# Optimization experiments

Measured on AMD Instinct MI355X. Metric: run time of the kernel, lower is better.

Reference implementation:

```python
import jax, jax.numpy as jnp
import numpy as np

N, E, F_IN, F_OUT = 20000, 8192, 128, 128


def setup_inputs() -> dict:
    key = jax.random.key(0)
    k1, k2, k3, k4, k5 = jax.random.split(key, 5)
    x = jax.random.normal(k1, (N, F_IN), dtype=jnp.float32)
    H = jax.random.uniform(k2, (N, E), dtype=jnp.float32)
    W = jax.random.uniform(k3, (E,), dtype=jnp.float32)  # diagonal of hyperedge weight matrix
    lin_w = jax.random.normal(k4, (F_OUT, F_IN), dtype=jnp.float32) * (1.0 / np.sqrt(F_IN))
    lin_b = jax.random.normal(k5, (F_OUT,), dtype=jnp.float32) * 0.01
    return {"x": x, "H": H, "W": W, "lin_w": lin_w, "lin_b": lin_b}


def reference(x, H, W, lin_w, lin_b):
    # Degrees
    Dv = jnp.clip(jnp.sum(H, axis=1), 1.0, None)          # [N] node degrees
    De = jnp.clip(jnp.sum(H, axis=0), 1.0, None)          # [E] hyperedge degrees
    dv_inv_sqrt = Dv ** -0.5                               # diag(Dv^-1/2)
    de_inv = 1.0 / De                                      # diag(De^-1)
    # Linear projection of node features
    xw = x @ lin_w.T + lin_b                               # [N, F_OUT]
    # L @ xw computed right-to-left: Dv^-1/2 H W De^-1 H^T Dv^-1/2 xw
    t = H.T @ (dv_inv_sqrt[:, None] * xw)                  # [E, F_OUT]
    t = (W * de_inv)[:, None] * t                          # diagonal W and De^-1 scaling
    out = dv_inv_sqrt[:, None] * (H @ t)                   # [N, F_OUT]
    return jax.nn.gelu(out, approximate=False)             # torch F.gelu default = exact erf
```

## Files before the change

kernel.cpp:

```cpp
#include <hip/hip_runtime.h>
#include <math.h>

static constexpr int N = 20000;
static constexpr int E = 8192;
static constexpr int F = 128;
static constexpr int NP = 20480;
static constexpr int NP2 = 20096;
static constexpr int PREP_BLOCKS = 2048;
static constexpr int XW_BLOCKS = NP / 8;
static constexpr int KS_B = 8;
static constexpr int KS_C = 4;

typedef short bf16x8 __attribute__((ext_vector_type(8)));
typedef float f32x4 __attribute__((ext_vector_type(4)));

__device__ __forceinline__ float gelu_erf(float x) {
    return 0.5f * x * (1.0f + erff(x * 0.70710678118654752440f));
}
__device__ __forceinline__ unsigned f2bf(float f) {
    unsigned u = __float_as_uint(f);
    return (u + 0x7FFFu + ((u >> 16) & 1u)) >> 16;
}
__device__ __forceinline__ void gload16(const void* g, void* lds) {
    __builtin_amdgcn_global_load_lds(
        (const __attribute__((address_space(1))) unsigned int*)g,
        (__attribute__((address_space(3))) unsigned int*)lds, 16, 0, 0);
}

__global__ __launch_bounds__(256, 8) void k_prep(const float* __restrict__ H,
                                                 float* __restrict__ Dv,
                                                 ushort* __restrict__ Hbs) {
    __shared__ float rp[10][4];
    const int tid = threadIdx.x, lane = tid & 63, wid = tid >> 6;
    const int r0 = blockIdx.x * 10;
    if (r0 >= N) {
        uint4 z = make_uint4(0, 0, 0, 0);
        for (int r = 0; r < 10; ++r) {
            ushort* orow = Hbs + (size_t)(r0 + r) * E;
#pragma unroll
            for (int j = 0; j < 4; ++j) *(uint4*)(orow + (j * 256 + tid) * 8) = z;
        }
        return;
    }
    for (int r = 0; r < 10; ++r) {
        const float* row = H + (size_t)(r0 + r) * E;
        ushort* orow = Hbs + (size_t)(r0 + r) * E;
        float rs = 0.f;
#pragma unroll
        for (int j = 0; j < 4; ++j) {
            const float* base = row + (j * 256 + tid) * 8;
            float4 va = *(const float4*)(base);
            float4 vb = *(const float4*)(base + 4);
            rs += (va.x + va.y) + (va.z + va.w);
            rs += (vb.x + vb.y) + (vb.z + vb.w);
            uint4 o;
            o.x = f2bf(va.x) | (f2bf(va.y) << 16);
            o.y = f2bf(va.z) | (f2bf(va.w) << 16);
            o.z = f2bf(vb.x) | (f2bf(vb.y) << 16);
            o.w = f2bf(vb.z) | (f2bf(vb.w) << 16);
            *(uint4*)(orow + (j * 256 + tid) * 8) = o;
        }
#pragma unroll
        for (int off = 32; off > 0; off >>= 1) rs += __shfl_xor(rs, off, 64);
        if (lane == 0) rp[r][wid] = rs;
    }
    __syncthreads();
    if (tid < 10) Dv[r0 + tid] = rp[tid][0] + rp[tid][1] + rp[tid][2] + rp[tid][3];
}

__global__ __launch_bounds__(256) void k_xw(const float* __restrict__ x,
                                            const float* __restrict__ lin_w,
                                            const float* __restrict__ lin_b,
                                            const float* __restrict__ Dv,
                                            ushort* __restrict__ yT) {
    __shared__ __align__(16) char smem[4096];
    const int tid = threadIdx.x;
    const int r0 = blockIdx.x * 8;
    if (r0 >= N) {
        if (tid < 128) {
            uint4 z = make_uint4(0, 0, 0, 0);
            *(uint4*)(yT + (size_t)tid * NP + r0) = z;
        }
        return;
    }
    float* xs = (float*)smem;
#pragma unroll
    for (int c = 0; c < 4; ++c) {
        int lin = c * 256 + tid;
        xs[lin] = x[(size_t)r0 * F + lin];
    }
    __syncthreads();
    const int f = tid & 127, half = tid >> 7;
    float b = lin_b[f];
    float a0 = b, a1 = b, a2 = b, a3 = b;
    const float* xr = xs + (half * 4) * F;
    const float* lwr = lin_w + (size_t)f * F;
#pragma unroll 4
    for (int k = 0; k < F; k += 4) {
        float4 lw = *(const float4*)(lwr + k);
        a0 += xr[0 * F + k] * lw.x; a0 += xr[0 * F + k + 1] * lw.y;
        a0 += xr[0 * F + k + 2] * lw.z; a0 += xr[0 * F + k + 3] * lw.w;
        a1 += xr[1 * F + k] * lw.x; a1 += xr[1 * F + k + 1] * lw.y;
        a1 += xr[1 * F + k + 2] * lw.z; a1 += xr[1 * F + k + 3] * lw.w;
        a2 += xr[2 * F + k] * lw.x; a2 += xr[2 * F + k + 1] * lw.y;
        a2 += xr[2 * F + k + 2] * lw.z; a2 += xr[2 * F + k + 3] * lw.w;
        a3 += xr[3 * F + k] * lw.x; a3 += xr[3 * F + k + 1] * lw.y;
        a3 += xr[3 * F + k + 2] * lw.z; a3 += xr[3 * F + k + 3] * lw.w;
    }
    const int rb = r0 + half * 4;
    a0 *= rsqrtf(fmaxf(Dv[rb + 0], 1.f));
    a1 *= rsqrtf(fmaxf(Dv[rb + 1], 1.f));
    a2 *= rsqrtf(fmaxf(Dv[rb + 2], 1.f));
    a3 *= rsqrtf(fmaxf(Dv[rb + 3], 1.f));
    __syncthreads();
    ushort* tile = (ushort*)smem;
    tile[(half * 4 + 0) * F + f] = (ushort)f2bf(a0);
    tile[(half * 4 + 1) * F + f] = (ushort)f2bf(a1);
    tile[(half * 4 + 2) * F + f] = (ushort)f2bf(a2);
    tile[(half * 4 + 3) * F + f] = (ushort)f2bf(a3);
    __syncthreads();
    if (tid < 128) {
        unsigned u[4];
#pragma unroll
        for (int qq = 0; qq < 4; ++qq) {
            ushort lo = tile[(qq * 2 + 0) * F + tid];
            ushort hi = tile[(qq * 2 + 1) * F + tid];
            u[qq] = (unsigned)lo | ((unsigned)hi << 16);
        }
        uint4 o = make_uint4(u[0], u[1], u[2], u[3]);
        *(uint4*)(yT + (size_t)tid * NP + r0) = o;
    }
}

__global__ void k_tst(const float* __restrict__ tB, const float* __restrict__ DeP2,
                      const float* __restrict__ W, ushort* __restrict__ tsT) {
    __shared__ __align__(16) char tl[8192];
    int tid = threadIdx.x;
    int r0 = (blockIdx.x >> 1) * 64;
    int c0 = (blockIdx.x & 1) * 64;
#pragma unroll
    for (int c = 0; c < 4; ++c) {
        int lin = c * 256 + tid;
        int row = lin >> 4, ch = lin & 15;
        size_t base = (size_t)(r0 + row) * F + c0 + ch * 4;
        float4 v = make_float4(0.f, 0.f, 0.f, 0.f);
#pragma unroll
        for (int ks = 0; ks < KS_B; ++ks) {
            float4 p = *(const float4*)(tB + (size_t)ks * E * F + base);
            v.x += p.x; v.y += p.y; v.z += p.z; v.w += p.w;
        }
        float d = 0.f;
#pragma unroll
        for (int ks = 0; ks < KS_B; ++ks) d += DeP2[(size_t)ks * E + r0 + row];
        float s = W[r0 + row] / fmaxf(d, 1.f);
        ushort4 b;
        b.x = (ushort)f2bf(v.x * s); b.y = (ushort)f2bf(v.y * s);
        b.z = (ushort)f2bf(v.z * s); b.w = (ushort)f2bf(v.w * s);
        int key = ((row ^ (row >> 3)) & 7) << 4;
        *(ushort4*)(tl + row * 128 + ((ch * 8) ^ key)) = b;
    }
    __syncthreads();
#pragma unroll
    for (int c = 0; c < 2; ++c) {
        int lin = c * 256 + tid;
        int fl = lin >> 3, vch = lin & 7;
        unsigned u[4];
#pragma unroll
        for (int qq = 0; qq < 4; ++qq) {
            int r1 = vch * 8 + qq * 2, r2 = r1 + 1;
            ushort a = *(const ushort*)(tl + r1 * 128 + ((fl * 2) ^ (((r1 ^ (r1 >> 3)) & 7) << 4)));
            ushort b = *(const ushort*)(tl + r2 * 128 + ((fl * 2) ^ (((r2 ^ (r2 >> 3)) & 7) << 4)));
            u[qq] = (unsigned)a | ((unsigned)b << 16);
        }
        uint4 o = make_uint4(u[0], u[1], u[2], u[3]);
        *(uint4*)(tsT + (size_t)(c0 + fl) * E + r0 + vch * 8) = o;
    }
}

__global__ __launch_bounds__(256) void k_gemmB(const ushort* __restrict__ Hbs,
                                               const ushort* __restrict__ yT,
                                               float* __restrict__ tB,
                                               float* __restrict__ DeP2) {
    __shared__ __align__(16) char lA[2][16384];
    __shared__ __align__(16) char lB[2][16384];
    const int tid = threadIdx.x;
    const int sw = (blockIdx.x & 7) * 64 + (blockIdx.x >> 3);
    const int m0 = (sw & 63) * 128;
    const int ks = sw >> 6;
    const int k0 = ks * 2560;
    const int lane = tid & 63, w = tid >> 6;
    const int wm = (w & 1) * 64, wn = (w >> 1) * 64;
    const int lrow = lane & 15, g16 = (lane >> 4) * 16;
    const int NSTEP = 40;

    const int vq = tid >> 4;
    const int e8 = (tid & 15) * 8;
    const ushort* pa = Hbs + (size_t)(k0 + vq * 4) * E + m0 + e8;
    const int abase = e8 * 128 + ((vq * 8) ^ ((tid & 7) << 4));

    const int row8 = lane >> 3, ch8 = lane & 7;
    const ushort* gB = yT + (size_t)(w * 32 + row8) * NP + k0 + ((ch8 ^ row8) * 8);
    const int ldstB = w * 32 * 128;

    int aoff[4][2], boff[4][2];
#pragma unroll
    for (int f = 0; f < 4; ++f)
#pragma unroll
        for (int kk = 0; kk < 2; ++kk) {
            int ma = wm + f * 16 + lrow;
            aoff[f][kk] = ma * 128 + (((kk * 64) + g16) ^ (((ma >> 3) & 7) << 4));
            int nb = wn + f * 16 + lrow;
            boff[f][kk] = nb * 128 + (((kk * 64) + g16) ^ ((nb & 7) << 4));
        }

    f32x4 zero4 = {0.f, 0.f, 0.f, 0.f};
    f32x4 acc[4][4];
    f32x4 deacc[4];
    const short oneb = (short)0x3F80;
    bf16x8 ones = {oneb, oneb, oneb, oneb, oneb, oneb, oneb, oneb};
#pragma unroll
    for (int i = 0; i < 4; ++i) {
        deacc[i] = zero4;
#pragma unroll
        for (int j = 0; j < 4; ++j) acc[i][j] = zero4;
    }

    uint4 ra[4];
#pragma unroll
    for (int r = 0; r < 4; ++r) ra[r] = *(const uint4*)(pa + (size_t)r * E);
    {
        const ushort* u0 = (const ushort*)&ra[0];
        const ushort* u1 = (const ushort*)&ra[1];
        const ushort* u2 = (const ushort*)&ra[2];
        const ushort* u3 = (const ushort*)&ra[3];
#pragma unroll
        for (int i = 0; i < 8; ++i) {
            uint2 wv;
            wv.x = (unsigned)u0[i] | ((unsigned)u1[i] << 16);
            wv.y = (unsigned)u2[i] | ((unsigned)u3[i] << 16);
            *(uint2*)(lA[0] + abase + i * 128) = wv;
        }
#pragma unroll
        for (int i = 0; i < 4; ++i)
            gload16(gB + (size_t)i * 8 * NP, lB[0] + ldstB + i * 1024);
    }
    pa += (size_t)64 * E;
#pragma unroll
    for (int r = 0; r < 4; ++r) ra[r] = *(const uint4*)(pa + (size_t)r * E);
    __syncthreads();

    for (int kt = 0; kt < NSTEP; ++kt) {
        const int cur = kt & 1;
        if (kt + 1 < NSTEP) {
            const ushort* u0 = (const ushort*)&ra[0];
            const ushort* u1 = (const ushort*)&ra[1];
            const ushort* u2 = (const ushort*)&ra[2];
            const ushort* u3 = (const ushort*)&ra[3];
#pragma unroll
            for (int i = 0; i < 8; ++i) {
                uint2 wv;
                wv.x = (unsigned)u0[i] | ((unsigned)u1[i] << 16);
                wv.y = (unsigned)u2[i] | ((unsigned)u3[i] << 16);
                *(uint2*)(lA[cur ^ 1] + abase + i * 128) = wv;
            }
            const int koff = (kt + 1) * 64;
#pragma unroll
            for (int i = 0; i < 4; ++i)
                gload16(gB + (size_t)i * 8 * NP + koff, lB[cur ^ 1] + ldstB + i * 1024);
        }
        if (kt + 2 < NSTEP) {
            pa += (size_t)64 * E;
#pragma unroll
            for (int r = 0; r < 4; ++r) ra[r] = *(const uint4*)(pa + (size_t)r * E);
        }
#pragma unroll
        for (int kk = 0; kk < 2; ++kk) {
            bf16x8 av[4], bv[4];
#pragma unroll
            for (int f = 0; f < 4; ++f) av[f] = *(const bf16x8*)(lA[cur] + aoff[f][kk]);
#pragma unroll
            for (int f = 0; f < 4; ++f) bv[f] = *(const bf16x8*)(lB[cur] + boff[f][kk]);
#pragma unroll
            for (int i = 0; i < 4; ++i)
                deacc[i] = __builtin_amdgcn_mfma_f32_16x16x32_bf16(av[i], ones, deacc[i], 0, 0, 0);
#pragma unroll
            for (int i = 0; i < 4; ++i)
#pragma unroll
                for (int j = 0; j < 4; ++j)
                    acc[i][j] = __builtin_amdgcn_mfma_f32_16x16x32_bf16(av[i], bv[j], acc[i][j], 0, 0, 0);
        }
        if (kt + 1 < NSTEP) __syncthreads();
    }
    float* plane = tB + (size_t)ks * E * F;
    const int orow = (lane >> 4) * 4, ocol = lane & 15;
#pragma unroll
    for (int i = 0; i < 4; ++i)
#pragma unroll
        for (int j = 0; j < 4; ++j) {
            int gm = m0 + wm + i * 16 + orow;
            int gn = wn + j * 16 + ocol;
#pragma unroll
            for (int q = 0; q < 4; ++q)
                plane[(size_t)(gm + q) * F + gn] = acc[i][j][q];
        }
    if (w < 2 && ocol == 0) {
        float* dep = DeP2 + (size_t)ks * E + m0 + wm + orow;
#pragma unroll
        for (int i = 0; i < 4; ++i)
            *(f32x4*)(dep + i * 16) = deacc[i];
    }
}

__global__ __launch_bounds__(256) void k_gemmC(const ushort* __restrict__ Hbs,
                                               const ushort* __restrict__ tsT,
                                               float* __restrict__ C2P) {
    __shared__ __align__(16) char lA[2][16384];
    __shared__ __align__(16) char lB[2][16384];
    const int tid = threadIdx.x;
    const int qq_ = 78, rr_ = 4;
    const int xcd = blockIdx.x & 7, idx = blockIdx.x >> 3;
    const int sw = (xcd < rr_ ? xcd * (qq_ + 1) : rr_ * (qq_ + 1) + (xcd - rr_) * qq_) + idx;
    const int m0 = (sw % 157) * 128;
    const int ks = sw / 157;
    const int k0 = ks * 2048;
    const int lane = tid & 63, w = tid >> 6;
    const int wm = (w & 1) * 64, wn = (w >> 1) * 64;
    const int lrow = lane & 15, g16 = (lane >> 4) * 16;
    const int NSTEP = 32;

    const int row8 = lane >> 3, ch8 = lane & 7;
    const ushort* gA = Hbs + (size_t)(m0 + w * 32 + row8) * E + k0 + ((ch8 ^ row8) * 8);
    const ushort* gB = tsT + (size_t)(w * 32 + row8) * E + k0 + ((ch8 ^ row8) * 8);
    const int ldst = w * 32 * 128;

    int aoff[4][2], boff[4][2];
#pragma unroll
    for (int f = 0; f < 4; ++f)
#pragma unroll
        for (int kk = 0; kk < 2; ++kk) {
            int ma = wm + f * 16 + lrow;
            aoff[f][kk] = ma * 128 + (((kk * 64) + g16) ^ ((ma & 7) << 4));
            int nb = wn + f * 16 + lrow;
            boff[f][kk] = nb * 128 + (((kk * 64) + g16) ^ ((nb & 7) << 4));
        }

    f32x4 zero4 = {0.f, 0.f, 0.f, 0.f};
    f32x4 acc[4][4];
#pragma unroll
    for (int i = 0; i < 4; ++i)
#pragma unroll
        for (int j = 0; j < 4; ++j) acc[i][j] = zero4;

#pragma unroll
    for (int i = 0; i < 4; ++i) {
        gload16(gA + (size_t)i * 8 * E, lA[0] + ldst + i * 1024);
        gload16(gB + (size_t)i * 8 * E, lB[0] + ldst + i * 1024);
    }
    __syncthreads();

    for (int kt = 0; kt < NSTEP; ++kt) {
        const int cur = kt & 1;
        if (kt + 1 < NSTEP) {
            const int koff = (kt + 1) * 64;
#pragma unroll
            for (int i = 0; i < 4; ++i) {
                gload16(gA + (size_t)i * 8 * E + koff, lA[cur ^ 1] + ldst + i * 1024);
                gload16(gB + (size_t)i * 8 * E + koff, lB[cur ^ 1] + ldst + i * 1024);
            }
        }
#pragma unroll
        for (int kk = 0; kk < 2; ++kk) {
            bf16x8 av[4], bv[4];
#pragma unroll
            for (int f = 0; f < 4; ++f) av[f] = *(const bf16x8*)(lA[cur] + aoff[f][kk]);
#pragma unroll
            for (int f = 0; f < 4; ++f) bv[f] = *(const bf16x8*)(lB[cur] + boff[f][kk]);
#pragma unroll
            for (int i = 0; i < 4; ++i)
#pragma unroll
                for (int j = 0; j < 4; ++j)
                    acc[i][j] = __builtin_amdgcn_mfma_f32_16x16x32_bf16(av[i], bv[j], acc[i][j], 0, 0, 0);
        }
        if (kt + 1 < NSTEP) __syncthreads();
    }
    float* plane = C2P + (size_t)ks * NP2 * F;
    const int orow = (lane >> 4) * 4, ocol = lane & 15;
#pragma unroll
    for (int i = 0; i < 4; ++i)
#pragma unroll
        for (int j = 0; j < 4; ++j) {
            int gm = m0 + wm + i * 16 + orow;
            int gn = wn + j * 16 + ocol;
#pragma unroll
            for (int q = 0; q < 4; ++q)
                plane[(size_t)(gm + q) * F + gn] = acc[i][j][q];
        }
}

__global__ void k_fin_out(const float* __restrict__ C2P, const float* __restrict__ Dv,
                          float* __restrict__ out) {
    int i4 = blockIdx.x * 256 + threadIdx.x;
    if (i4 < N * F / 4) {
        int n = i4 >> 5;
        float s = rsqrtf(fmaxf(Dv[n], 1.f));
        float4 v = make_float4(0.f, 0.f, 0.f, 0.f);
#pragma unroll
        for (int ks = 0; ks < KS_C; ++ks) {
            float4 p = reinterpret_cast<const float4*>(C2P + (size_t)ks * NP2 * F)[i4];
            v.x += p.x; v.y += p.y; v.z += p.z; v.w += p.w;
        }
        float4 o;
        o.x = gelu_erf(s * v.x);
        o.y = gelu_erf(s * v.y);
        o.z = gelu_erf(s * v.z);
        o.w = gelu_erf(s * v.w);
        reinterpret_cast<float4*>(out)[i4] = o;
    }
}

extern "C" void kernel_launch(void* const* d_in, const int* in_sizes, int n_in,
                              void* d_out, int out_size, void* d_ws, size_t ws_size,
                              hipStream_t stream) {
    const float* x     = (const float*)d_in[0];
    const float* H     = (const float*)d_in[1];
    const float* W     = (const float*)d_in[2];
    const float* lin_w = (const float*)d_in[3];
    const float* lin_b = (const float*)d_in[4];
    float* out = (float*)d_out;

    char* ws = (char*)d_ws;
    ushort* Hbs  = (ushort*)ws;
    ushort* yT   = (ushort*)(ws + 335544320);
    float*  tB   = (float*) (ws + 340787200);
    ushort* tsT  = (ushort*)(ws + 374341632);
    float*  C2P  = (float*) (ws + 376438784);
    float*  DeP2 = (float*) (ws + 417595392);
    float*  Dv   = (float*) (ws + 417857536);

    k_prep<<<PREP_BLOCKS, 256, 0, stream>>>(H, Dv, Hbs);
    k_xw<<<XW_BLOCKS, 256, 0, stream>>>(x, lin_w, lin_b, Dv, yT);
    k_gemmB<<<64 * KS_B, 256, 0, stream>>>(Hbs, yT, tB, DeP2);
    k_tst<<<(E / 64) * 2, 256, 0, stream>>>(tB, DeP2, W, tsT);
    k_gemmC<<<157 * KS_C, 256, 0, stream>>>(Hbs, tsT, C2P);
    k_fin_out<<<(N * F / 4 + 255) / 256, 256, 0, stream>>>(C2P, Dv, out);
}
```

Baseline: 455.1 us.

## Drop bf16 copy of H and convert fp32 H on the fly in GEMMs

Replaces the prep kernel that wrote a bf16 copy of H with a row-sum-only kernel, and has both GEMM kernels load fp32 H directly, converting to bf16 in registers before storing to LDS. This removes the large bf16 write and its workspace. In exchange, each GEMM reads twice as many bytes of H, and gemmC loses its direct global-to-LDS async loads in favour of register staging with conversion work.

```diff
diff --git a/kernel.cpp b/kernel.cpp
--- a/kernel.cpp
+++ b/kernel.cpp
@@ -6,7 +6,6 @@
 static constexpr int F = 128;
 static constexpr int NP = 20480;
 static constexpr int NP2 = 20096;
-static constexpr int PREP_BLOCKS = 2048;
 static constexpr int XW_BLOCKS = NP / 8;
 static constexpr int KS_B = 8;
 static constexpr int KS_C = 4;
@@ -27,38 +26,18 @@
         (__attribute__((address_space(3))) unsigned int*)lds, 16, 0, 0);
 }
 
-__global__ __launch_bounds__(256, 8) void k_prep(const float* __restrict__ H,
-                                                 float* __restrict__ Dv,
-                                                 ushort* __restrict__ Hbs) {
+__global__ __launch_bounds__(256) void k_dv(const float* __restrict__ H,
+                                            float* __restrict__ Dv) {
     __shared__ float rp[10][4];
     const int tid = threadIdx.x, lane = tid & 63, wid = tid >> 6;
     const int r0 = blockIdx.x * 10;
-    if (r0 >= N) {
-        uint4 z = make_uint4(0, 0, 0, 0);
-        for (int r = 0; r < 10; ++r) {
-            ushort* orow = Hbs + (size_t)(r0 + r) * E;
-#pragma unroll
-            for (int j = 0; j < 4; ++j) *(uint4*)(orow + (j * 256 + tid) * 8) = z;
-        }
-        return;
-    }
     for (int r = 0; r < 10; ++r) {
         const float* row = H + (size_t)(r0 + r) * E;
-        ushort* orow = Hbs + (size_t)(r0 + r) * E;
         float rs = 0.f;
 #pragma unroll
-        for (int j = 0; j < 4; ++j) {
-            const float* base = row + (j * 256 + tid) * 8;
-            float4 va = *(const float4*)(base);
-            float4 vb = *(const float4*)(base + 4);
-            rs += (va.x + va.y) + (va.z + va.w);
-            rs += (vb.x + vb.y) + (vb.z + vb.w);
-            uint4 o;
-            o.x = f2bf(va.x) | (f2bf(va.y) << 16);
-            o.y = f2bf(va.z) | (f2bf(va.w) << 16);
-            o.z = f2bf(vb.x) | (f2bf(vb.y) << 16);
-            o.w = f2bf(vb.z) | (f2bf(vb.w) << 16);
-            *(uint4*)(orow + (j * 256 + tid) * 8) = o;
+        for (int j = 0; j < 8; ++j) {
+            float4 v = *(const float4*)(row + j * 1024 + tid * 4);
+            rs += (v.x + v.y) + (v.z + v.w);
         }
 #pragma unroll
         for (int off = 32; off > 0; off >>= 1) rs += __shfl_xor(rs, off, 64);
@@ -177,7 +156,7 @@
     }
 }
 
-__global__ __launch_bounds__(256) void k_gemmB(const ushort* __restrict__ Hbs,
+__global__ __launch_bounds__(256) void k_gemmB(const float* __restrict__ H,
                                                const ushort* __restrict__ yT,
                                                float* __restrict__ tB,
                                                float* __restrict__ DeP2) {
@@ -195,7 +174,8 @@
 
     const int vq = tid >> 4;
     const int e8 = (tid & 15) * 8;
-    const ushort* pa = Hbs + (size_t)(k0 + vq * 4) * E + m0 + e8;
+    int vcur = k0 + vq * 4;
+    const float* paH = H + (size_t)vcur * E + m0 + e8;
     const int abase = e8 * 128 + ((vq * 8) ^ ((tid & 7) << 4));
 
     const int row8 = lane >> 3, ch8 = lane & 7;
@@ -225,53 +205,55 @@
         for (int j = 0; j < 4; ++j) acc[i][j] = zero4;
     }
 
-    uint4 ra[4];
-#pragma unroll
-    for (int r = 0; r < 4; ++r) ra[r] = *(const uint4*)(pa + (size_t)r * E);
-    {
-        const ushort* u0 = (const ushort*)&ra[0];
-        const ushort* u1 = (const ushort*)&ra[1];
-        const ushort* u2 = (const ushort*)&ra[2];
-        const ushort* u3 = (const ushort*)&ra[3];
-#pragma unroll
-        for (int i = 0; i < 8; ++i) {
-            uint2 wv;
-            wv.x = (unsigned)u0[i] | ((unsigned)u1[i] << 16);
-            wv.y = (unsigned)u2[i] | ((unsigned)u3[i] << 16);
-            *(uint2*)(lA[0] + abase + i * 128) = wv;
-        }
-#pragma unroll
-        for (int i = 0; i < 4; ++i)
-            gload16(gB + (size_t)i * 8 * NP, lB[0] + ldstB + i * 1024);
-    }
-    pa += (size_t)64 * E;
-#pragma unroll
-    for (int r = 0; r < 4; ++r) ra[r] = *(const uint4*)(pa + (size_t)r * E);
+    float4 ra[4][2];
+#define LOAD_A()                                                            \
+    {                                                                       \
+        _Pragma("unroll")                                                   \
+        for (int r = 0; r < 4; ++r) {                                       \
+            bool ok = (vcur + r) < N;                                       \
+            const float* p = ok ? (paH + (size_t)r * E) : H;                \
+            float4 va = *(const float4*)(p);                                \
+            float4 vb = *(const float4*)(p + 4);                            \
+            if (!ok) { va = make_float4(0.f,0.f,0.f,0.f); vb = va; }        \
+            ra[r][0] = va; ra[r][1] = vb;                                   \
+        }                                                                   \
+    }
+#define WRITE_A(buf)                                                        \
+    {                                                                       \
+        _Pragma("unroll")                                                   \
+        for (int i = 0; i < 8; ++i) {                                       \
+            unsigned u0 = f2bf(((const float*)&ra[0][i >> 2])[i & 3]);      \
+            unsigned u1 = f2bf(((const float*)&ra[1][i >> 2])[i & 3]);      \
+            unsigned u2 = f2bf(((const float*)&ra[2][i >> 2])[i & 3]);      \
+            unsigned u3 = f2bf(((const float*)&ra[3][i >> 2])[i & 3]);      \
+            uint2 wv;                                                       \
+            wv.x = u0 | (u1 << 16);                                         \
+            wv.y = u2 | (u3 << 16);                                         \
+            *(uint2*)(lA[buf] + abase + i * 128) = wv;                      \
+        }                                                                   \
+    }
+
+    LOAD_A();
+    WRITE_A(0);
+#pragma unroll
+    for (int i = 0; i < 4; ++i)
+        gload16(gB + (size_t)i * 8 * NP, lB[0] + ldstB + i * 1024);
+    vcur += 64; paH += (size_t)64 * E;
+    LOAD_A();
     __syncthreads();
 
     for (int kt = 0; kt < NSTEP; ++kt) {
         const int cur = kt & 1;
         if (kt + 1 < NSTEP) {
-            const ushort* u0 = (const ushort*)&ra[0];
-            const ushort* u1 = (const ushort*)&ra[1];
-            const ushort* u2 = (const ushort*)&ra[2];
-            const ushort* u3 = (const ushort*)&ra[3];
-#pragma unroll
-            for (int i = 0; i < 8; ++i) {
-                uint2 wv;
-                wv.x = (unsigned)u0[i] | ((unsigned)u1[i] << 16);
-                wv.y = (unsigned)u2[i] | ((unsigned)u3[i] << 16);
-                *(uint2*)(lA[cur ^ 1] + abase + i * 128) = wv;
-            }
+            WRITE_A(cur ^ 1);
             const int koff = (kt + 1) * 64;
 #pragma unroll
             for (int i = 0; i < 4; ++i)
                 gload16(gB + (size_t)i * 8 * NP + koff, lB[cur ^ 1] + ldstB + i * 1024);
         }
         if (kt + 2 < NSTEP) {
-            pa += (size_t)64 * E;
-#pragma unroll
-            for (int r = 0; r < 4; ++r) ra[r] = *(const uint4*)(pa + (size_t)r * E);
+            vcur += 64; paH += (size_t)64 * E;
+            LOAD_A();
         }
 #pragma unroll
         for (int kk = 0; kk < 2; ++kk) {
@@ -291,6 +273,8 @@
         }
         if (kt + 1 < NSTEP) __syncthreads();
     }
+#undef LOAD_A
+#undef WRITE_A
     float* plane = tB + (size_t)ks * E * F;
     const int orow = (lane >> 4) * 4, ocol = lane & 15;
 #pragma unroll
@@ -311,7 +295,7 @@
     }
 }
 
-__global__ __launch_bounds__(256) void k_gemmC(const ushort* __restrict__ Hbs,
+__global__ __launch_bounds__(256) void k_gemmC(const float* __restrict__ H,
                                                const ushort* __restrict__ tsT,
                                                float* __restrict__ C2P) {
     __shared__ __align__(16) char lA[2][16384];
@@ -328,8 +312,18 @@
     const int lrow = lane & 15, g16 = (lane >> 4) * 16;
     const int NSTEP = 32;
 
+    int arow[4], awoff[4];
+    const float* gAp[4];
+#pragma unroll
+    for (int c = 0; c < 4; ++c) {
+        int lin = c * 256 + tid;
+        int row = lin >> 3, ch = lin & 7;
+        arow[c] = m0 + row;
+        bool ok = arow[c] < N;
+        gAp[c] = H + (size_t)(ok ? arow[c] : 0) * E + k0 + ch * 8;
+        awoff[c] = row * 128 + ((ch * 16) ^ ((row & 7) << 4));
+    }
     const int row8 = lane >> 3, ch8 = lane & 7;
-    const ushort* gA = Hbs + (size_t)(m0 + w * 32 + row8) * E + k0 + ((ch8 ^ row8) * 8);
     const ushort* gB = tsT + (size_t)(w * 32 + row8) * E + k0 + ((ch8 ^ row8) * 8);
     const int ldst = w * 32 * 128;
 
@@ -351,23 +345,48 @@
 #pragma unroll
         for (int j = 0; j < 4; ++j) acc[i][j] = zero4;
 
-#pragma unroll
-    for (int i = 0; i < 4; ++i) {
-        gload16(gA + (size_t)i * 8 * E, lA[0] + ldst + i * 1024);
+    float4 rc[4][2];
+#define LOAD_AC(koff)                                                       \
+    {                                                                       \
+        _Pragma("unroll")                                                   \
+        for (int c = 0; c < 4; ++c) {                                       \
+            float4 va = *(const float4*)(gAp[c] + (koff));                  \
+            float4 vb = *(const float4*)(gAp[c] + (koff) + 4);              \
+            if (arow[c] >= N) { va = make_float4(0.f,0.f,0.f,0.f); vb = va; } \
+            rc[c][0] = va; rc[c][1] = vb;                                   \
+        }                                                                   \
+    }
+#define WRITE_AC(buf)                                                       \
+    {                                                                       \
+        _Pragma("unroll")                                                   \
+        for (int c = 0; c < 4; ++c) {                                       \
+            uint4 o;                                                        \
+            o.x = f2bf(rc[c][0].x) | (f2bf(rc[c][0].y) << 16);              \
+            o.y = f2bf(rc[c][0].z) | (f2bf(rc[c][0].w) << 16);              \
+            o.z = f2bf(rc[c][1].x) | (f2bf(rc[c][1].y) << 16);              \
+            o.w = f2bf(rc[c][1].z) | (f2bf(rc[c][1].w) << 16);              \
+            *(uint4*)(lA[buf] + awoff[c]) = o;                              \
+        }                                                                   \
+    }
+
+    LOAD_AC(0);
+    WRITE_AC(0);
+#pragma unroll
+    for (int i = 0; i < 4; ++i)
         gload16(gB + (size_t)i * 8 * E, lB[0] + ldst + i * 1024);
-    }
+    LOAD_AC(64);
     __syncthreads();
 
     for (int kt = 0; kt < NSTEP; ++kt) {
         const int cur = kt & 1;
         if (kt + 1 < NSTEP) {
+            WRITE_AC(cur ^ 1);
             const int koff = (kt + 1) * 64;
 #pragma unroll
-            for (int i = 0; i < 4; ++i) {
-                gload16(gA + (size_t)i * 8 * E + koff, lA[cur ^ 1] + ldst + i * 1024);
+            for (int i = 0; i < 4; ++i)
                 gload16(gB + (size_t)i * 8 * E + koff, lB[cur ^ 1] + ldst + i * 1024);
-            }
-        }
+        }
+        if (kt + 2 < NSTEP) LOAD_AC((kt + 2) * 64);
 #pragma unroll
         for (int kk = 0; kk < 2; ++kk) {
             bf16x8 av[4], bv[4];
@@ -383,6 +402,8 @@
         }
         if (kt + 1 < NSTEP) __syncthreads();
     }
+#undef LOAD_AC
+#undef WRITE_AC
     float* plane = C2P + (size_t)ks * NP2 * F;
     const int orow = (lane >> 4) * 4, ocol = lane & 15;
 #pragma unroll
@@ -429,18 +450,17 @@
     float* out = (float*)d_out;
 
     char* ws = (char*)d_ws;
-    ushort* Hbs  = (ushort*)ws;
-    ushort* yT   = (ushort*)(ws + 335544320);
-    float*  tB   = (float*) (ws + 340787200);
-    ushort* tsT  = (ushort*)(ws + 374341632);
-    float*  C2P  = (float*) (ws + 376438784);
-    float*  DeP2 = (float*) (ws + 417595392);
-    float*  Dv   = (float*) (ws + 417857536);
-
-    k_prep<<<PREP_BLOCKS, 256, 0, stream>>>(H, Dv, Hbs);
+    ushort* yT   = (ushort*)ws;
+    float*  tB   = (float*) (ws + 5242880);
+    ushort* tsT  = (ushort*)(ws + 38797312);
+    float*  C2P  = (float*) (ws + 40894464);
+    float*  DeP2 = (float*) (ws + 82051072);
+    float*  Dv   = (float*) (ws + 82313216);
+
+    k_dv<<<N / 10, 256, 0, stream>>>(H, Dv);
     k_xw<<<XW_BLOCKS, 256, 0, stream>>>(x, lin_w, lin_b, Dv, yT);
-    k_gemmB<<<64 * KS_B, 256, 0, stream>>>(Hbs, yT, tB, DeP2);
+    k_gemmB<<<64 * KS_B, 256, 0, stream>>>(H, yT, tB, DeP2);
     k_tst<<<(E / 64) * 2, 256, 0, stream>>>(tB, DeP2, W, tsT);
-    k_gemmC<<<157 * KS_C, 256, 0, stream>>>(Hbs, tsT, C2P);
+    k_gemmC<<<157 * KS_C, 256, 0, stream>>>(H, tsT, C2P);
     k_fin_out<<<(N * F / 4 + 255) / 256, 256, 0, stream>>>(C2P, Dv, out);
 }
```

New measurement: 506.4 us. 11.3% more time.
